# Performance work log

Measured on AMD Instinct MI355X. Metric: run time of the kernel, lower is better.

## Reference

```python
import jax, jax.numpy as jnp
import numpy as np

N_NODES = 50000
N_EDGES = 800000
SIZES = [128, 256, 256, 128]
EPS = 1e-5


def setup_inputs() -> dict:
    key = jax.random.key(0)
    ks = jax.random.split(key, 2 + 5 * (len(SIZES) - 1))
    inp = {
        "x": jax.random.normal(ks[0], (N_NODES, SIZES[0]), dtype=jnp.float32),
        "edge_index": jax.random.randint(ks[1], (2, N_EDGES), 0, N_NODES, dtype=jnp.int64),
    }
    k = 2
    for i, (fin, fout) in enumerate(zip(SIZES[:-1], SIZES[1:])):
        scale = 1.0 / np.sqrt(fin)
        inp[f"W{i}"] = jax.random.normal(ks[k], (fout, fin), dtype=jnp.float32) * scale; k += 1
        inp[f"b{i}"] = jnp.zeros((fout,), dtype=jnp.float32)
        inp[f"g{i}"] = jnp.ones((fout,), dtype=jnp.float32)   # LayerNorm weight
        inp[f"be{i}"] = jnp.zeros((fout,), dtype=jnp.float32)  # LayerNorm bias
        inp[f"a{i}"] = jnp.full((1,), 0.25, dtype=jnp.float32)  # PReLU slope
        k += 3  # keep key consumption deterministic
    return inp


def _gcn_conv(x, src, dst, dinv, W, b):
    # GCNConv: h = x @ W^T; aggregate norm(src,dst) * h[src] into dst; add bias.
    h = x @ W.T  # [N, F_out]
    norm = dinv[src] * dinv[dst]  # [E+N]
    msg = norm[:, None] * h[src]  # [E+N, F_out]
    return jax.ops.segment_sum(msg, dst, num_segments=N_NODES) + b


def _layernorm_graph(x, g, be):
    # PyG LayerNorm(mode='graph'): normalize over all nodes and channels.
    mu = x.mean()
    xc = x - mu
    var = (xc * xc).mean()
    return xc / jnp.sqrt(var + EPS) * g + be


def _prelu(x, a):
    return jnp.where(x >= 0, x, a * x)


def reference(x, edge_index, W0, b0, g0, be0, a0, W1, b1, g1, be1, a1, W2, b2, g2, be2, a2):
    loop = jnp.arange(N_NODES, dtype=edge_index.dtype)
    src = jnp.concatenate([edge_index[0], loop])  # add self-loops
    dst = jnp.concatenate([edge_index[1], loop])
    deg = jax.ops.segment_sum(jnp.ones_like(dst, dtype=x.dtype), dst, num_segments=N_NODES)
    dinv = jax.lax.rsqrt(deg)  # deg >= 1 due to self-loops
    params = [(W0, b0, g0, be0, a0), (W1, b1, g1, be1, a1), (W2, b2, g2, be2, a2)]
    for W, b, g, be, a in params:
        x = _gcn_conv(x, src, dst, dinv, W, b)
        x = _layernorm_graph(x, g, be)
        x = _prelu(x, a)
    return x
```

## Files before the change

kernel.cpp:

```cpp
#include <hip/hip_runtime.h>

#define N_NODES 50000
#define N_EDGES 800000
#define EPS 1e-5f

typedef __attribute__((ext_vector_type(8))) short bf16x8;
typedef __attribute__((ext_vector_type(4))) float f32x4;
typedef __attribute__((ext_vector_type(4))) unsigned short us4;

__device__ __forceinline__ unsigned short f2b(float f) {
    union { float f; unsigned int u; } v; v.f = f;
    unsigned int r = v.u + 0x7fffu + ((v.u >> 16) & 1u);
    return (unsigned short)(r >> 16);
}
__device__ __forceinline__ float b2f(unsigned short b) {
    union { unsigned int u; float f; } v; v.u = ((unsigned int)b) << 16;
    return v.f;
}


#define RED_BUCKETS 64
#define RED_FLOATS_PER_LAYER (RED_BUCKETS * 16)


#define CV_NX (N_NODES * 128 / 4)
#define CV_N0 (256 * 128 / 4)
#define CV_N1 (256 * 256 / 4)
#define CV_N2 (128 * 256 / 4)

__global__ void prep_kernel(const float* __restrict__ x0, const float* __restrict__ W0,
                            const float* __restrict__ W1, const float* __restrict__ W2,
                            unsigned short* __restrict__ xb, unsigned short* __restrict__ wb0,
                            unsigned short* __restrict__ wb1, unsigned short* __restrict__ wb2,
                            int* __restrict__ deg, int* __restrict__ fill,
                            float* __restrict__ red) {
    int i = blockIdx.x * 256 + threadIdx.x;
    if (i < N_NODES) { deg[i] = 0; fill[i] = 0; }
    if (i < 3 * RED_FLOATS_PER_LAYER) red[i] = 0.f;
    int j = i;
    if (j < CV_NX) {
        float4 v = reinterpret_cast<const float4*>(x0)[j];
        int n = j >> 5;
        int col0 = (j & 31) * 4;
        us4 o;
        o[0] = f2b(v.x); o[1] = f2b(v.y); o[2] = f2b(v.z); o[3] = f2b(v.w);
        *reinterpret_cast<us4*>(xb + ((size_t)(col0 >> 5) * N_NODES + n) * 32 + (col0 & 31)) = o;
        return;
    }
    const float* s;
    unsigned short* d;
    if ((j -= CV_NX) < CV_N0) { s = W0; d = wb0; }
    else if ((j -= CV_N0) < CV_N1) { s = W1; d = wb1; }
    else if ((j -= CV_N1) < CV_N2) { s = W2; d = wb2; }
    else return;
    float4 v = reinterpret_cast<const float4*>(s)[j];
    us4 o;
    o[0] = f2b(v.x); o[1] = f2b(v.y); o[2] = f2b(v.z); o[3] = f2b(v.w);
    reinterpret_cast<us4*>(d)[j] = o;
}


__global__ void count_kernel(const int* __restrict__ dst, int* __restrict__ deg, int e) {
    for (int i = blockIdx.x * blockDim.x + threadIdx.x; i < e; i += gridDim.x * blockDim.x)
        atomicAdd(&deg[dst[i]], 1);
}

__global__ void scan1_kernel(const int* __restrict__ deg, float* __restrict__ dinv,
                             int* __restrict__ bsum, int n) {
    int i = blockIdx.x * 256 + threadIdx.x;
    int v = (i < n) ? deg[i] : 0;
    if (i < n) dinv[i] = rsqrtf((float)(v + 1));
    int t = v;
    #pragma unroll
    for (int off = 1; off < 64; off <<= 1) t += __shfl_xor(t, off);
    __shared__ int wsum[4];
    int wid = threadIdx.x >> 6, lane = threadIdx.x & 63;
    if (lane == 0) wsum[wid] = t;
    __syncthreads();
    if (threadIdx.x == 0) bsum[blockIdx.x] = wsum[0] + wsum[1] + wsum[2] + wsum[3];
}

__global__ void scan2_kernel(const int* __restrict__ bsum, int* __restrict__ bpre, int nb) {
    __shared__ int sm[256];
    int t = threadIdx.x;
    sm[t] = (t < nb) ? bsum[t] : 0;
    __syncthreads();
    #pragma unroll
    for (int d = 1; d < 256; d <<= 1) {
        int x = (t >= d) ? sm[t - d] : 0;
        __syncthreads();
        sm[t] += x;
        __syncthreads();
    }
    bpre[t] = (t > 0) ? sm[t - 1] : 0;
}

__global__ void scan3_kernel(const int* __restrict__ deg, const int* __restrict__ bpre,
                             int* __restrict__ off, int n) {
    __shared__ int sm[256];
    int t = threadIdx.x;
    int i = blockIdx.x * 256 + t;
    int v = (i < n) ? deg[i] : 0;
    sm[t] = v;
    __syncthreads();
    #pragma unroll
    for (int d = 1; d < 256; d <<= 1) {
        int x = (t >= d) ? sm[t - d] : 0;
        __syncthreads();
        sm[t] += x;
        __syncthreads();
    }
    if (i < n) off[i + 1] = sm[t] + bpre[blockIdx.x];
    if (i == 0) off[0] = 0;
}

__global__ void scatter_kernel(const int* __restrict__ src, const int* __restrict__ dst,
                               const int* __restrict__ coff, int* __restrict__ fill,
                               const float* __restrict__ dinv,
                               unsigned int* __restrict__ epack, int e) {
    for (int i = blockIdx.x * blockDim.x + threadIdx.x; i < e; i += gridDim.x * blockDim.x) {
        int d = dst[i];
        int s = src[i];
        int pos = coff[d] + atomicAdd(&fill[d], 1);
        epack[pos] = ((unsigned int)f2b(dinv[s] * dinv[d]) << 16) | (unsigned int)s;
    }
}


template<int BN, bool TRANSFORM, bool ADD_BIAS, bool FUSE_RED>
__device__ __forceinline__ void gemm_body(
    const unsigned short* __restrict__ Xin, const unsigned short* __restrict__ Wb,
    const float* __restrict__ bias, const float* __restrict__ redin,
    const float* __restrict__ gw, const float* __restrict__ bw,
    const float* __restrict__ asl, float* __restrict__ redout,
    unsigned short* __restrict__ Hout, int M, int K, float inv_count) {
    constexpr int FR_N = BN / 64;
    __shared__ unsigned short xs[2][64 * 32];
    int tid = threadIdx.x;
    int wid = tid >> 6, lane = tid & 63;
    int l16 = lane & 15, kg = lane >> 4;
    int srow = tid >> 2, sblk = tid & 3;
    int m0 = blockIdx.x * 64;
    int colbase = wid * (BN / 4);

    float mu = 0.f, rstd = 0.f, alpha = 0.f;
    if (TRANSFORM) {
        float s = redin[lane * 16], s2 = redin[lane * 16 + 1];
        #pragma unroll
        for (int off = 1; off < 64; off <<= 1) { s += __shfl_xor(s, off); s2 += __shfl_xor(s2, off); }
        mu = s * inv_count;
        rstd = rsqrtf(s2 * inv_count - mu * mu + EPS);
        alpha = asl[0];
    }

    int gmr = m0 + srow;
    bool inm = (gmr < M);
    const unsigned short* xrow = Xin + (size_t)gmr * 32 + sblk * 8;
    unsigned short* xdst = &xs[0][srow * 32 + ((sblk ^ (srow & 3)) * 8)];

    auto stage = [&](int k0, int buf) {
        bf16x8 xv = {};
        if (inm) {
            bf16x8 u = *reinterpret_cast<const bf16x8*>(xrow + (size_t)(k0 >> 5) * N_NODES * 32);
            if (TRANSFORM) {
                int f0 = k0 + sblk * 8;
                float ga[8], ba[8];
                *reinterpret_cast<float4*>(&ga[0]) = *reinterpret_cast<const float4*>(gw + f0);
                *reinterpret_cast<float4*>(&ga[4]) = *reinterpret_cast<const float4*>(gw + f0 + 4);
                *reinterpret_cast<float4*>(&ba[0]) = *reinterpret_cast<const float4*>(bw + f0);
                *reinterpret_cast<float4*>(&ba[4]) = *reinterpret_cast<const float4*>(bw + f0 + 4);
                #pragma unroll
                for (int i = 0; i < 8; ++i) {
                    float A = rstd * ga[i];
                    float B = ba[i] - mu * A;
                    float v = fmaf(b2f((unsigned short)u[i]), A, B);
                    v = fmaf(fminf(v, 0.f), alpha - 1.0f, v);
                    xv[i] = (short)f2b(v);
                }
            } else {
                xv = u;
            }
        }
        *reinterpret_cast<bf16x8*>(xdst + buf * (64 * 32)) = xv;
    };

    stage(0, 0);
    f32x4 acc[4][FR_N] = {};
    int nsteps = K / 32;
    for (int s = 0; s < nsteps; ++s) {
        __syncthreads();
        int k0 = s * 32;
        if (s + 1 < nsteps) stage(k0 + 32, (s + 1) & 1);
        bf16x8 b[FR_N];
        #pragma unroll
        for (int j = 0; j < FR_N; ++j)
            b[j] = *reinterpret_cast<const bf16x8*>(
                Wb + (size_t)(colbase + j * 16 + l16) * K + k0 + kg * 8);
        const unsigned short* xbuf = xs[s & 1];
        bf16x8 a[4];
        #pragma unroll
        for (int i = 0; i < 4; ++i) {
            int ar = i * 16 + l16;
            a[i] = *reinterpret_cast<const bf16x8*>(xbuf + ar * 32 + ((kg ^ (ar & 3)) * 8));
        }
        #pragma unroll
        for (int i = 0; i < 4; ++i)
            #pragma unroll
            for (int j = 0; j < FR_N; ++j)
                acc[i][j] = __builtin_amdgcn_mfma_f32_16x16x32_bf16(b[j], a[i], acc[i][j], 0, 0, 0);
    }

    float bsel[FR_N][4];
    if (ADD_BIAS) {
        #pragma unroll
        for (int j = 0; j < FR_N; ++j)
            *reinterpret_cast<float4*>(bsel[j]) =
                *reinterpret_cast<const float4*>(bias + colbase + j * 16 + kg * 4);
    }
    float s = 0.f, s2 = 0.f;
    #pragma unroll
    for (int i = 0; i < 4; ++i) {
        int row = m0 + i * 16 + l16;
        if (row < M) {
            #pragma unroll
            for (int j = 0; j < FR_N; ++j) {
                int col = colbase + j * 16 + kg * 4;
                us4 o;
                #pragma unroll
                for (int r = 0; r < 4; ++r) {
                    float v = acc[i][j][r] + (ADD_BIAS ? bsel[j][r] : 0.f);
                    if (FUSE_RED) { s += v; s2 += v * v; }
                    o[r] = f2b(v);
                }
                *reinterpret_cast<us4*>(
                    Hout + ((size_t)(col >> 5) * N_NODES + row) * 32 + (col & 31)) = o;
            }
        }
    }
    if (FUSE_RED) {
        #pragma unroll
        for (int off = 1; off < 64; off <<= 1) { s += __shfl_xor(s, off); s2 += __shfl_xor(s2, off); }
        if (lane == 0) {
            int bkt = (blockIdx.x & (RED_BUCKETS - 1)) * 16;
            atomicAdd(&redout[bkt], s);
            atomicAdd(&redout[bkt + 1], s2);
        }
    }
}


template<int COLS, bool ADD_BIAS, bool FUSE_RED>
__device__ __forceinline__ void agg_body(
    const unsigned short* __restrict__ Hb, const int* __restrict__ coff,
    const unsigned int* __restrict__ epack, const float* __restrict__ dinv,
    const float* __restrict__ bias, unsigned short* __restrict__ Y,
    float* __restrict__ red) {
    constexpr int CHUNKS = COLS / 32;
    int chunk = blockIdx.x % CHUNKS;
    int nodeblk = blockIdx.x / CHUNKS;
    int t = threadIdx.x;
    int node = nodeblk * 64 + (t >> 2);
    int rl = t & 3;
    bool active = node < N_NODES;
    const unsigned short* base = Hb + (size_t)chunk * N_NODES * 32 + rl * 8;
    int s0 = 0, s1 = 0;
    float wc = 0.f;
    if (active) {
        s0 = coff[node]; s1 = coff[node + 1];
        float di = dinv[node];
        wc = di * di;
    }
    float acc[8] = {};
    int k = s0 - 1;
    bf16x8 vc = {};
    bool have = active;
    if (have) vc = *reinterpret_cast<const bf16x8*>(base + (size_t)node * 32);
    while (__any(have)) {
        int k2 = k + 1;
        bool have2 = have && (k2 < s1);
        float wn = 0.f;
        bf16x8 vn = {};
        if (have2) {
            unsigned int u = epack[k2];
            wn = b2f((unsigned short)(u >> 16));
            vn = *reinterpret_cast<const bf16x8*>(base + (size_t)(u & 0xffffu) * 32);
        }
        if (have) {
            #pragma unroll
            for (int i = 0; i < 8; ++i) acc[i] += wc * b2f((unsigned short)vc[i]);
        }
        k = k2; wc = wn; vc = vn; have = have2;
    }
    if (ADD_BIAS && active) {
        #pragma unroll
        for (int i = 0; i < 8; ++i) acc[i] += bias[chunk * 32 + rl * 8 + i];
    }
    if (FUSE_RED) {
        float s = 0.f, s2 = 0.f;
        #pragma unroll
        for (int i = 0; i < 8; ++i) { s += acc[i]; s2 += acc[i] * acc[i]; }
        #pragma unroll
        for (int off = 1; off < 64; off <<= 1) { s += __shfl_xor(s, off); s2 += __shfl_xor(s2, off); }
        if ((t & 63) == 0) {
            int bkt = (blockIdx.x & (RED_BUCKETS - 1)) * 16;
            atomicAdd(&red[bkt], s);
            atomicAdd(&red[bkt + 1], s2);
        }
    }
    if (active) {
        bf16x8 o;
        #pragma unroll
        for (int i = 0; i < 8; ++i) o[i] = (short)f2b(acc[i]);
        __builtin_nontemporal_store(
            o, reinterpret_cast<bf16x8*>(Y + ((size_t)chunk * N_NODES + node) * 32 + rl * 8));
    }
}


__global__ __launch_bounds__(256) void gemm_l0(const unsigned short* X, const unsigned short* W,
                                               const float* bias, float* redout,
                                               unsigned short* H, int M, int K, float ic) {
    gemm_body<256, false, true, true>(X, W, bias, nullptr, nullptr, nullptr, nullptr, redout, H, M, K, ic);
}
__global__ __launch_bounds__(256) void gemm_l1(const unsigned short* X, const unsigned short* W,
                                               const float* redin, const float* gw, const float* bw,
                                               const float* asl, unsigned short* H, int M, int K, float ic) {
    gemm_body<256, true, false, false>(X, W, nullptr, redin, gw, bw, asl, nullptr, H, M, K, ic);
}
__global__ __launch_bounds__(256) void gemm_l2(const unsigned short* X, const unsigned short* W,
                                               const float* redin, const float* gw, const float* bw,
                                               const float* asl, unsigned short* H, int M, int K, float ic) {
    gemm_body<128, true, false, false>(X, W, nullptr, redin, gw, bw, asl, nullptr, H, M, K, ic);
}
__global__ void agg_l0(const unsigned short* Hb, const int* coff, const unsigned int* ep,
                       const float* dinv, unsigned short* Y) {
    agg_body<128, false, false>(Hb, coff, ep, dinv, nullptr, Y, nullptr);
}
__global__ void agg_l1(const unsigned short* Hb, const int* coff, const unsigned int* ep,
                       const float* dinv, const float* bias, unsigned short* Y, float* red) {
    agg_body<256, true, true>(Hb, coff, ep, dinv, bias, Y, red);
}
__global__ void agg_l2(const unsigned short* Hb, const int* coff, const unsigned int* ep,
                       const float* dinv, const float* bias, unsigned short* Y, float* red) {
    agg_body<128, true, true>(Hb, coff, ep, dinv, bias, Y, red);
}


__global__ void norm_final(const unsigned short* __restrict__ Yb, const float* __restrict__ red,
                           const float* __restrict__ g, const float* __restrict__ be,
                           const float* __restrict__ a, float* __restrict__ X,
                           float inv_count) {
    int lane = threadIdx.x & 63;
    float s = red[lane * 16], s2 = red[lane * 16 + 1];
    #pragma unroll
    for (int off = 1; off < 64; off <<= 1) { s += __shfl_xor(s, off); s2 += __shfl_xor(s2, off); }
    float mu = s * inv_count;
    float rstd = rsqrtf(s2 * inv_count - mu * mu + EPS);
    float alpha = a[0];
    int total = N_NODES * 128 / 8;
    for (int i = blockIdx.x * blockDim.x + threadIdx.x; i < total; i += gridDim.x * blockDim.x) {
        bf16x8 v = reinterpret_cast<const bf16x8*>(Yb)[i];
        int c = i / (N_NODES * 4);
        int rem = i - c * (N_NODES * 4);
        int n = rem >> 2;
        int r = rem & 3;
        int f0 = c * 32 + r * 8;
        float o[8];
        #pragma unroll
        for (int j = 0; j < 8; ++j) {
            float t = (b2f((unsigned short)v[j]) - mu) * rstd * g[f0 + j] + be[f0 + j];
            o[j] = t >= 0.f ? t : alpha * t;
        }
        float* xp = X + (size_t)n * 128 + f0;
        *reinterpret_cast<float4*>(xp) = make_float4(o[0], o[1], o[2], o[3]);
        *reinterpret_cast<float4*>(xp + 4) = make_float4(o[4], o[5], o[6], o[7]);
    }
}


extern "C" void kernel_launch(void* const* d_in, const int* in_sizes, int n_in,
                              void* d_out, int out_size, void* d_ws, size_t ws_size,
                              hipStream_t stream) {
    const float* x0 = (const float*)d_in[0];
    const int* ei = (const int*)d_in[1];
    const float* W[3] = {(const float*)d_in[2], (const float*)d_in[7], (const float*)d_in[12]};
    const float* bb[3] = {(const float*)d_in[3], (const float*)d_in[8], (const float*)d_in[13]};
    const float* gg[3] = {(const float*)d_in[4], (const float*)d_in[9], (const float*)d_in[14]};
    const float* be[3] = {(const float*)d_in[5], (const float*)d_in[10], (const float*)d_in[15]};
    const float* aa[3] = {(const float*)d_in[6], (const float*)d_in[11], (const float*)d_in[16]};

    char* ws = (char*)d_ws;
    size_t o = 0;
    auto alloc = [&](size_t bytes) {
        void* p = ws + o;
        o = (o + bytes + 255) & ~(size_t)255;
        return p;
    };
    int* deg = (int*)alloc(N_NODES * 4);
    int* fill = (int*)alloc(N_NODES * 4);
    int* coff = (int*)alloc((N_NODES + 1) * 4);
    unsigned int* epack = (unsigned int*)alloc((size_t)N_EDGES * 4);
    float* dinv = (float*)alloc(N_NODES * 4);
    int* bsum = (int*)alloc(256 * 4);
    int* bpre = (int*)alloc(256 * 4);
    float* red = (float*)alloc(3 * RED_FLOATS_PER_LAYER * 4);
    unsigned short* Wb0 = (unsigned short*)alloc(256 * 128 * 2);
    unsigned short* Wb1 = (unsigned short*)alloc(256 * 256 * 2);
    unsigned short* Wb2 = (unsigned short*)alloc(128 * 256 * 2);
    unsigned short* xb = (unsigned short*)alloc((size_t)N_NODES * 128 * 2);
    unsigned short* hb = (unsigned short*)alloc((size_t)N_NODES * 256 * 2);
    unsigned short* yb = (unsigned short*)alloc((size_t)N_NODES * 256 * 2);

    const int* e_src = ei;
    const int* e_dst = ei + N_EDGES;
    int nb = (N_NODES + 255) / 256;

    int cvtot = CV_NX + CV_N0 + CV_N1 + CV_N2;
    prep_kernel<<<(cvtot + 255) / 256, 256, 0, stream>>>(x0, W[0], W[1], W[2], xb, Wb0, Wb1, Wb2,
                                                         deg, fill, red);
    count_kernel<<<2048, 256, 0, stream>>>(e_dst, deg, N_EDGES);
    scan1_kernel<<<nb, 256, 0, stream>>>(deg, dinv, bsum, N_NODES);
    scan2_kernel<<<1, 256, 0, stream>>>(bsum, bpre, nb);
    scan3_kernel<<<nb, 256, 0, stream>>>(deg, bpre, coff, N_NODES);
    scatter_kernel<<<2048, 256, 0, stream>>>(e_src, e_dst, coff, fill, dinv, epack, N_EDGES);

    int gm = (N_NODES + 63) / 64;
    float ic256 = 1.0f / (N_NODES * 256.0f);
    float ic128 = 1.0f / (N_NODES * 128.0f);

    agg_l0<<<gm * 4, 256, 0, stream>>>(xb, coff, epack, dinv, hb);
    gemm_l0<<<gm, 256, 0, stream>>>(hb, Wb0, bb[0], red + 0, yb, N_NODES, 128, ic256);

    gemm_l1<<<gm, 256, 0, stream>>>(yb, Wb1, red + 0, gg[0], be[0], aa[0], hb, N_NODES, 256, ic256);
    agg_l1<<<gm * 8, 256, 0, stream>>>(hb, coff, epack, dinv, bb[1], yb, red + RED_FLOATS_PER_LAYER);

    gemm_l2<<<gm, 256, 0, stream>>>(yb, Wb2, red + RED_FLOATS_PER_LAYER, gg[1], be[1], aa[1], hb,
                                    N_NODES, 256, ic256);
    agg_l2<<<gm * 4, 256, 0, stream>>>(hb, coff, epack, dinv, bb[2], yb,
                                       red + 2 * RED_FLOATS_PER_LAYER);

    norm_final<<<2048, 256, 0, stream>>>(yb, red + 2 * RED_FLOATS_PER_LAYER, gg[2], be[2], aa[2],
                                         (float*)d_out, ic128);
}
```

Baseline: 328.6 us.

## Split each node's edge list across four thread groups in aggregation

The CSR aggregation now assigns 16 threads per node instead of 4, so four groups each walk every fourth edge (the self-loop is folded in as a virtual edge before the first). Partial sums are combined with cross-lane shuffles and only group 0 adds the bias, contributes to the LayerNorm statistics and writes the output. Edge metadata loads become nontemporal. The intent is more memory-level parallelism on the irregular gathers and less serial latency per node, at the cost of four times as many blocks, extra shuffle reductions and idle lanes on low-degree nodes.

```diff
diff --git a/kernel.cpp b/kernel.cpp
--- a/kernel.cpp
+++ b/kernel.cpp
@@ -259,29 +259,36 @@
     int chunk = blockIdx.x % CHUNKS;
     int nodeblk = blockIdx.x / CHUNKS;
     int t = threadIdx.x;
-    int node = nodeblk * 64 + (t >> 2);
-    int rl = t & 3;
+    int node = nodeblk * 16 + (t >> 4);
+    int sub = t & 15;
+    int g = sub >> 2;
+    int rl = sub & 3;
     bool active = node < N_NODES;
     const unsigned short* base = Hb + (size_t)chunk * N_NODES * 32 + rl * 8;
     int s0 = 0, s1 = 0;
+    float di = 0.f;
+    if (active) { s0 = coff[node]; s1 = coff[node + 1]; di = dinv[node]; }
+    float acc[8] = {};
+
+    int k = s0 - 1 + g;
     float wc = 0.f;
-    if (active) {
-        s0 = coff[node]; s1 = coff[node + 1];
-        float di = dinv[node];
-        wc = di * di;
-    }
-    float acc[8] = {};
-    int k = s0 - 1;
     bf16x8 vc = {};
-    bool have = active;
-    if (have) vc = *reinterpret_cast<const bf16x8*>(base + (size_t)node * 32);
+    bool have = active && (k < s1);
+    if (have) {
+        if (k < s0) { wc = di * di; vc = *reinterpret_cast<const bf16x8*>(base + (size_t)node * 32); }
+        else {
+            unsigned int u = __builtin_nontemporal_load(&epack[k]);
+            wc = b2f((unsigned short)(u >> 16));
+            vc = *reinterpret_cast<const bf16x8*>(base + (size_t)(u & 0xffffu) * 32);
+        }
+    }
     while (__any(have)) {
-        int k2 = k + 1;
+        int k2 = k + 4;
         bool have2 = have && (k2 < s1);
         float wn = 0.f;
         bf16x8 vn = {};
         if (have2) {
-            unsigned int u = epack[k2];
+            unsigned int u = __builtin_nontemporal_load(&epack[k2]);
             wn = b2f((unsigned short)(u >> 16));
             vn = *reinterpret_cast<const bf16x8*>(base + (size_t)(u & 0xffffu) * 32);
         }
@@ -291,14 +298,22 @@
         }
         k = k2; wc = wn; vc = vn; have = have2;
     }
-    if (ADD_BIAS && active) {
+
+    #pragma unroll
+    for (int off = 4; off <= 8; off <<= 1) {
+        #pragma unroll
+        for (int i = 0; i < 8; ++i) acc[i] += __shfl_xor(acc[i], off);
+    }
+    if (ADD_BIAS && active && g == 0) {
         #pragma unroll
         for (int i = 0; i < 8; ++i) acc[i] += bias[chunk * 32 + rl * 8 + i];
     }
     if (FUSE_RED) {
         float s = 0.f, s2 = 0.f;
-        #pragma unroll
-        for (int i = 0; i < 8; ++i) { s += acc[i]; s2 += acc[i] * acc[i]; }
+        if (g == 0) {
+            #pragma unroll
+            for (int i = 0; i < 8; ++i) { s += acc[i]; s2 += acc[i] * acc[i]; }
+        }
         #pragma unroll
         for (int off = 1; off < 64; off <<= 1) { s += __shfl_xor(s, off); s2 += __shfl_xor(s2, off); }
         if ((t & 63) == 0) {
@@ -307,7 +322,7 @@
             atomicAdd(&red[bkt + 1], s2);
         }
     }
-    if (active) {
+    if (active && g == 0) {
         bf16x8 o;
         #pragma unroll
         for (int i = 0; i < 8; ++i) o[i] = (short)f2b(acc[i]);
@@ -425,19 +440,21 @@
     scatter_kernel<<<2048, 256, 0, stream>>>(e_src, e_dst, coff, fill, dinv, epack, N_EDGES);
 
     int gm = (N_NODES + 63) / 64;
+    int nblk16 = (N_NODES + 15) / 16;
     float ic256 = 1.0f / (N_NODES * 256.0f);
     float ic128 = 1.0f / (N_NODES * 128.0f);
 
-    agg_l0<<<gm * 4, 256, 0, stream>>>(xb, coff, epack, dinv, hb);
+    agg_l0<<<nblk16 * 4, 256, 0, stream>>>(xb, coff, epack, dinv, hb);
     gemm_l0<<<gm, 256, 0, stream>>>(hb, Wb0, bb[0], red + 0, yb, N_NODES, 128, ic256);
 
     gemm_l1<<<gm, 256, 0, stream>>>(yb, Wb1, red + 0, gg[0], be[0], aa[0], hb, N_NODES, 256, ic256);
-    agg_l1<<<gm * 8, 256, 0, stream>>>(hb, coff, epack, dinv, bb[1], yb, red + RED_FLOATS_PER_LAYER);
+    agg_l1<<<nblk16 * 8, 256, 0, stream>>>(hb, coff, epack, dinv, bb[1], yb,
+                                           red + RED_FLOATS_PER_LAYER);
 
     gemm_l2<<<gm, 256, 0, stream>>>(yb, Wb2, red + RED_FLOATS_PER_LAYER, gg[1], be[1], aa[1], hb,
                                     N_NODES, 256, ic256);
-    agg_l2<<<gm * 4, 256, 0, stream>>>(hb, coff, epack, dinv, bb[2], yb,
-                                       red + 2 * RED_FLOATS_PER_LAYER);
+    agg_l2<<<nblk16 * 4, 256, 0, stream>>>(hb, coff, epack, dinv, bb[2], yb,
+                                           red + 2 * RED_FLOATS_PER_LAYER);
 
     norm_final<<<2048, 256, 0, stream>>>(yb, red + 2 * RED_FLOATS_PER_LAYER, gg[2], be[2], aa[2],
                                          (float*)d_out, ic128);
```

After: 387.0 us. 1.18x slower.

## Sort nodes by degree for aggregation and prefetch edge indices one step ahead

Applied to the files above, without the earlier changes.

Builds a degree histogram and counting-sort permutation of nodes so each aggregation wavefront processes nodes of similar degree, which cuts divergence from the __any loop running to the wavefront's maximum degree. It also software-pipelines the edge-index load one iteration further ahead, so the next index is in hand before the gather. In exchange it adds a permute kernel and histogram atomics, an indirect perm lookup, and scattered output rows, since the permutation breaks the locality of row writes.

```diff
diff --git a/kernel.cpp b/kernel.cpp
--- a/kernel.cpp
+++ b/kernel.cpp
@@ -33,9 +33,11 @@
                             unsigned short* __restrict__ xb, unsigned short* __restrict__ wb0,
                             unsigned short* __restrict__ wb1, unsigned short* __restrict__ wb2,
                             int* __restrict__ deg, int* __restrict__ fill,
+                            int* __restrict__ hist, int* __restrict__ fill2,
                             float* __restrict__ red) {
     int i = blockIdx.x * 256 + threadIdx.x;
     if (i < N_NODES) { deg[i] = 0; fill[i] = 0; }
+    if (i < 256) { hist[i] = 0; fill2[i] = 0; }
     if (i < 3 * RED_FLOATS_PER_LAYER) red[i] = 0.f;
     int j = i;
     if (j < CV_NX) {
@@ -66,10 +68,13 @@
 }
 
 __global__ void scan1_kernel(const int* __restrict__ deg, float* __restrict__ dinv,
-                             int* __restrict__ bsum, int n) {
+                             int* __restrict__ bsum, int* __restrict__ hist, int n) {
     int i = blockIdx.x * 256 + threadIdx.x;
     int v = (i < n) ? deg[i] : 0;
-    if (i < n) dinv[i] = rsqrtf((float)(v + 1));
+    if (i < n) {
+        dinv[i] = rsqrtf((float)(v + 1));
+        atomicAdd(&hist[v < 255 ? v : 255], 1);
+    }
     int t = v;
     #pragma unroll
     for (int off = 1; off < 64; off <<= 1) t += __shfl_xor(t, off);
@@ -80,7 +85,8 @@
     if (threadIdx.x == 0) bsum[blockIdx.x] = wsum[0] + wsum[1] + wsum[2] + wsum[3];
 }
 
-__global__ void scan2_kernel(const int* __restrict__ bsum, int* __restrict__ bpre, int nb) {
+__global__ void scan2_kernel(const int* __restrict__ bsum, int* __restrict__ bpre, int nb,
+                             const int* __restrict__ hist, int* __restrict__ binpre) {
     __shared__ int sm[256];
     int t = threadIdx.x;
     sm[t] = (t < nb) ? bsum[t] : 0;
@@ -93,6 +99,17 @@
         __syncthreads();
     }
     bpre[t] = (t > 0) ? sm[t - 1] : 0;
+    __syncthreads();
+    sm[t] = hist[t];
+    __syncthreads();
+    #pragma unroll
+    for (int d = 1; d < 256; d <<= 1) {
+        int x = (t >= d) ? sm[t - d] : 0;
+        __syncthreads();
+        sm[t] += x;
+        __syncthreads();
+    }
+    binpre[t] = (t > 0) ? sm[t - 1] : 0;
 }
 
 __global__ void scan3_kernel(const int* __restrict__ deg, const int* __restrict__ bpre,
@@ -112,6 +129,16 @@
     }
     if (i < n) off[i + 1] = sm[t] + bpre[blockIdx.x];
     if (i == 0) off[0] = 0;
+}
+
+__global__ void permute_kernel(const int* __restrict__ deg, const int* __restrict__ binpre,
+                               int* __restrict__ fill2, int* __restrict__ perm, int n) {
+    int i = blockIdx.x * 256 + threadIdx.x;
+    if (i < n) {
+        int v = deg[i];
+        int b = v < 255 ? v : 255;
+        perm[binpre[b] + atomicAdd(&fill2[b], 1)] = i;
+    }
 }
 
 __global__ void scatter_kernel(const int* __restrict__ src, const int* __restrict__ dst,
@@ -253,15 +280,18 @@
 __device__ __forceinline__ void agg_body(
     const unsigned short* __restrict__ Hb, const int* __restrict__ coff,
     const unsigned int* __restrict__ epack, const float* __restrict__ dinv,
+    const int* __restrict__ perm,
     const float* __restrict__ bias, unsigned short* __restrict__ Y,
     float* __restrict__ red) {
     constexpr int CHUNKS = COLS / 32;
     int chunk = blockIdx.x % CHUNKS;
     int nodeblk = blockIdx.x / CHUNKS;
     int t = threadIdx.x;
-    int node = nodeblk * 64 + (t >> 2);
+    int nidx = nodeblk * 64 + (t >> 2);
     int rl = t & 3;
-    bool active = node < N_NODES;
+    bool active = nidx < N_NODES;
+    int node = 0;
+    if (active) node = perm[nidx];
     const unsigned short* base = Hb + (size_t)chunk * N_NODES * 32 + rl * 8;
     int s0 = 0, s1 = 0;
     float wc = 0.f;
@@ -271,25 +301,28 @@
         wc = di * di;
     }
     float acc[8] = {};
-    int k = s0 - 1;
     bf16x8 vc = {};
     bool have = active;
     if (have) vc = *reinterpret_cast<const bf16x8*>(base + (size_t)node * 32);
+    unsigned int u1 = 0;
+    if (active && s0 < s1) u1 = epack[s0];
+    int k = s0 - 1;
     while (__any(have)) {
-        int k2 = k + 1;
-        bool have2 = have && (k2 < s1);
+        int k1 = k + 1, k2 = k + 2;
+        bool have1 = have && (k1 < s1);
+        unsigned int u2 = 0;
+        if (have && k2 < s1) u2 = epack[k2];
         float wn = 0.f;
         bf16x8 vn = {};
-        if (have2) {
-            unsigned int u = epack[k2];
-            wn = b2f((unsigned short)(u >> 16));
-            vn = *reinterpret_cast<const bf16x8*>(base + (size_t)(u & 0xffffu) * 32);
+        if (have1) {
+            wn = b2f((unsigned short)(u1 >> 16));
+            vn = *reinterpret_cast<const bf16x8*>(base + (size_t)(u1 & 0xffffu) * 32);
         }
         if (have) {
             #pragma unroll
             for (int i = 0; i < 8; ++i) acc[i] += wc * b2f((unsigned short)vc[i]);
         }
-        k = k2; wc = wn; vc = vn; have = have2;
+        k = k1; wc = wn; vc = vn; u1 = u2; have = have1;
     }
     if (ADD_BIAS && active) {
         #pragma unroll
@@ -333,16 +366,18 @@
     gemm_body<128, true, false, false>(X, W, nullptr, redin, gw, bw, asl, nullptr, H, M, K, ic);
 }
 __global__ void agg_l0(const unsigned short* Hb, const int* coff, const unsigned int* ep,
-                       const float* dinv, unsigned short* Y) {
-    agg_body<128, false, false>(Hb, coff, ep, dinv, nullptr, Y, nullptr);
+                       const float* dinv, const int* perm, unsigned short* Y) {
+    agg_body<128, false, false>(Hb, coff, ep, dinv, perm, nullptr, Y, nullptr);
 }
 __global__ void agg_l1(const unsigned short* Hb, const int* coff, const unsigned int* ep,
-                       const float* dinv, const float* bias, unsigned short* Y, float* red) {
-    agg_body<256, true, true>(Hb, coff, ep, dinv, bias, Y, red);
+                       const float* dinv, const int* perm, const float* bias,
+                       unsigned short* Y, float* red) {
+    agg_body<256, true, true>(Hb, coff, ep, dinv, perm, bias, Y, red);
 }
 __global__ void agg_l2(const unsigned short* Hb, const int* coff, const unsigned int* ep,
-                       const float* dinv, const float* bias, unsigned short* Y, float* red) {
-    agg_body<128, true, true>(Hb, coff, ep, dinv, bias, Y, red);
+                       const float* dinv, const int* perm, const float* bias,
+                       unsigned short* Y, float* red) {
+    agg_body<128, true, true>(Hb, coff, ep, dinv, perm, bias, Y, red);
 }
 
 
@@ -403,6 +438,10 @@
     float* dinv = (float*)alloc(N_NODES * 4);
     int* bsum = (int*)alloc(256 * 4);
     int* bpre = (int*)alloc(256 * 4);
+    int* hist = (int*)alloc(256 * 4);
+    int* binpre = (int*)alloc(256 * 4);
+    int* fill2 = (int*)alloc(256 * 4);
+    int* perm = (int*)alloc(N_NODES * 4);
     float* red = (float*)alloc(3 * RED_FLOATS_PER_LAYER * 4);
     unsigned short* Wb0 = (unsigned short*)alloc(256 * 128 * 2);
     unsigned short* Wb1 = (unsigned short*)alloc(256 * 256 * 2);
@@ -417,26 +456,28 @@
 
     int cvtot = CV_NX + CV_N0 + CV_N1 + CV_N2;
     prep_kernel<<<(cvtot + 255) / 256, 256, 0, stream>>>(x0, W[0], W[1], W[2], xb, Wb0, Wb1, Wb2,
-                                                         deg, fill, red);
+                                                         deg, fill, hist, fill2, red);
     count_kernel<<<2048, 256, 0, stream>>>(e_dst, deg, N_EDGES);
-    scan1_kernel<<<nb, 256, 0, stream>>>(deg, dinv, bsum, N_NODES);
-    scan2_kernel<<<1, 256, 0, stream>>>(bsum, bpre, nb);
+    scan1_kernel<<<nb, 256, 0, stream>>>(deg, dinv, bsum, hist, N_NODES);
+    scan2_kernel<<<1, 256, 0, stream>>>(bsum, bpre, nb, hist, binpre);
     scan3_kernel<<<nb, 256, 0, stream>>>(deg, bpre, coff, N_NODES);
+    permute_kernel<<<nb, 256, 0, stream>>>(deg, binpre, fill2, perm, N_NODES);
     scatter_kernel<<<2048, 256, 0, stream>>>(e_src, e_dst, coff, fill, dinv, epack, N_EDGES);
 
     int gm = (N_NODES + 63) / 64;
     float ic256 = 1.0f / (N_NODES * 256.0f);
     float ic128 = 1.0f / (N_NODES * 128.0f);
 
-    agg_l0<<<gm * 4, 256, 0, stream>>>(xb, coff, epack, dinv, hb);
+    agg_l0<<<gm * 4, 256, 0, stream>>>(xb, coff, epack, dinv, perm, hb);
     gemm_l0<<<gm, 256, 0, stream>>>(hb, Wb0, bb[0], red + 0, yb, N_NODES, 128, ic256);
 
     gemm_l1<<<gm, 256, 0, stream>>>(yb, Wb1, red + 0, gg[0], be[0], aa[0], hb, N_NODES, 256, ic256);
-    agg_l1<<<gm * 8, 256, 0, stream>>>(hb, coff, epack, dinv, bb[1], yb, red + RED_FLOATS_PER_LAYER);
+    agg_l1<<<gm * 8, 256, 0, stream>>>(hb, coff, epack, dinv, perm, bb[1], yb,
+                                       red + RED_FLOATS_PER_LAYER);
 
     gemm_l2<<<gm, 256, 0, stream>>>(yb, Wb2, red + RED_FLOATS_PER_LAYER, gg[1], be[1], aa[1], hb,
                                     N_NODES, 256, ic256);
-    agg_l2<<<gm * 4, 256, 0, stream>>>(hb, coff, epack, dinv, bb[2], yb,
+    agg_l2<<<gm * 4, 256, 0, stream>>>(hb, coff, epack, dinv, perm, bb[2], yb,
                                        red + 2 * RED_FLOATS_PER_LAYER);
 
     norm_final<<<2048, 256, 0, stream>>>(yb, red + 2 * RED_FLOATS_PER_LAYER, gg[2], be[2], aa[2],
```

After: 622.9 us. 89.6% more time.
